# Kernel tuning notes

Measured on AMD Instinct MI355X. Metric: run time of the kernel, lower is better.

Reference implementation:

```python
import jax, jax.numpy as jnp
import numpy as np

ANCHORS = np.array([[4.63,1.97,1.74],[6.93,2.51,2.84],[6.37,2.85,3.19],[10.5,2.94,3.47],
                    [12.29,2.9,3.87],[0.5,2.53,0.98],[2.11,0.77,1.47],[1.7,0.6,1.28],
                    [0.73,0.67,1.77],[0.41,0.41,1.07]], dtype=np.float32)  # [10,3] nuScenes anchor sizes
BINS = 20          # anchor_size_bins
TEXT_DIM = 3 * BINS
NUM_PROPOSALS = 200
NMS_K = 3


def _vector_values():
    la = np.log(ANCHORS)
    return np.linspace(la.min() - 0.1, la.max() - 0.1, BINS).astype(np.float32)


def _anchor_vecs_normed():
    # soft_relu_bin_vectors: soft-bin log-anchors into BINS bins per dim, dim-major flatten
    vals = _vector_values()
    inc = vals[1] - vals[0]
    la = np.log(ANCHORS)                                      # [10,3]
    v = np.clip((la[:, :, None] - vals[None, None, :]) / inc, 0.0, 1.0)  # [10,3,BINS]
    v = v.reshape(10, TEXT_DIM)
    return (v / (1e-8 + np.linalg.norm(v, axis=1, keepdims=True))).astype(np.float32)


def conv2d(x, w, b=None):
    y = jax.lax.conv_general_dilated(x, w, (1, 1), 'SAME',
                                     dimension_numbers=('NCHW', 'OIHW', 'NCHW'))
    if b is not None:
        y = y + b[None, :, None, None]
    return y


def iou_sim_vec(a):
    # vectorized form of the triple-nested loop: prod over dims of min/max ratio
    mn = jnp.minimum(a[:, None, :], a[None, :, :])
    mx = jnp.maximum(a[:, None, :], a[None, :, :])
    return jnp.prod(mn / mx, axis=-1)                         # [10,10]


def setup_inputs() -> dict:
    key = jax.random.key(0)
    ks = jax.random.split(key, 8)
    B, Cin, hid, H, W = 2, 512, 128, 180, 180
    feats = jax.random.normal(ks[0], (B, Cin, H, W), jnp.float32)
    w_shared = jax.random.normal(ks[1], (hid, Cin, 3, 3), jnp.float32) * 0.02
    b_shared = jnp.zeros((hid,), jnp.float32)
    w_bb = jax.random.normal(ks[2], (hid, hid, 3, 3), jnp.float32) * 0.05
    gamma_bb = jnp.ones((hid,), jnp.float32)
    beta_bb = jnp.zeros((hid,), jnp.float32)
    w_hm = jax.random.normal(ks[3], (TEXT_DIM, hid, 3, 3), jnp.float32) * 0.05
    b_hm = jnp.zeros((TEXT_DIM,), jnp.float32)
    thr_scale = jnp.ones((1,), jnp.float32)                   # Threshold2d scale
    logit_scale = jnp.ones((1,), jnp.float32) * np.log(1.0 / 0.07)
    logit_bias = jnp.ones((1,), jnp.float32) * (-10.0)
    w_enc = jax.random.normal(ks[4], (hid, 3), jnp.float32) * 0.1  # Conv1d(3->hid, k=1)
    anchor_vecs = jnp.asarray(_anchor_vecs_normed())
    xs = jnp.arange(W, dtype=jnp.float32) + 0.5
    ys = jnp.arange(H, dtype=jnp.float32) + 0.5
    gy, gx = jnp.meshgrid(ys, xs, indexing='ij')
    bev_pos = jnp.stack([gx.reshape(-1), gy.reshape(-1)], axis=-1)  # [H*W, 2]
    return dict(feats=feats, w_shared=w_shared, b_shared=b_shared, w_bb=w_bb,
                gamma_bb=gamma_bb, beta_bb=beta_bb, w_hm=w_hm, b_hm=b_hm,
                thr_scale=thr_scale, logit_scale=logit_scale, logit_bias=logit_bias,
                w_enc=w_enc, anchor_vecs=anchor_vecs, bev_pos=bev_pos)


def reference(feats, w_shared, b_shared, w_bb, gamma_bb, beta_bb, w_hm, b_hm,
              thr_scale, logit_scale, logit_bias, w_enc, anchor_vecs, bev_pos):
    B, _, H, W = feats.shape
    # shared conv
    lidar_feat = conv2d(feats, w_shared, b_shared)            # [B,hid,H,W]
    # BasicBlock2D: conv + (inference) BN + ReLU
    x = conv2d(lidar_feat, w_bb)
    x = jax.nn.relu(x * gamma_bb[None, :, None, None] + beta_bb[None, :, None, None])
    # heatmap conv -> Threshold2d (sigmoid((x - thresholds) * scale))
    vec = conv2d(x, w_hm, b_hm)                               # [B,60,H,W]
    thresholds = jnp.asarray(np.tile(_vector_values(), 3))[None, :, None, None]
    vec = jax.nn.sigmoid((vec - thresholds) * thr_scale[0])
    # cosine sim vs normalized anchor bin-vectors -> per-class heatmap
    vecn = vec / (1e-8 + jnp.linalg.norm(vec, axis=1, keepdims=True))
    sim = jnp.einsum('bchw,kc->bkhw', vecn, anchor_vecs)      # [B,10,H,W]
    heatmap = jax.nn.sigmoid(logit_scale[0] * sim + logit_bias[0])
    # NMS: keep only local maxima within nms_kernel_size window
    local_max = jax.lax.reduce_window(heatmap, -jnp.inf, jax.lax.max,
                                      (1, 1, NMS_K, NMS_K), (1, 1, 1, 1), 'SAME')
    hm_nms = jnp.where(heatmap == local_max, heatmap, 0.0)
    # top-k proposals over classes x positions
    flat = hm_nms.reshape(B, -1)                              # [B, 10*H*W]
    top_scores, top_idx = jax.lax.top_k(flat, NUM_PROPOSALS)
    top_labels = top_idx // (H * W)                           # [B,P]
    top_pos = top_idx % (H * W)                               # [B,P]
    # gather proposal features, heatmap scores and bev positions
    hid = lidar_feat.shape[1]
    lidar_flat = lidar_feat.reshape(B, hid, H * W)
    idx_f = jnp.broadcast_to(top_pos[:, None, :], (B, hid, NUM_PROPOSALS))
    query_feat = jnp.take_along_axis(lidar_flat, idx_f, axis=2)  # [B,hid,P]
    hm_flat = heatmap.reshape(B, 10, H * W)
    idx_h = jnp.broadcast_to(top_pos[:, None, :], (B, 10, NUM_PROPOSALS))
    query_hm_score = jnp.take_along_axis(hm_flat, idx_h, axis=2)  # [B,10,P]
    query_pos = bev_pos[top_pos]                              # [B,P,2]
    # anchor value encoding (Conv1d(3->hid,k=1) on log-anchor sizes of top classes)
    top_anchor = jnp.log(jnp.asarray(ANCHORS))[top_labels]    # [B,P,3]
    query_feat = query_feat + jnp.einsum('cd,bpd->bcp', w_enc, top_anchor)
    sims = iou_sim_vec(jnp.asarray(ANCHORS))                  # [10,10] anchor IoU similarity
    return heatmap, top_scores, top_labels, query_feat, query_pos, query_hm_score, sims
```

## Files before the change

### kernel.cpp

```cpp
#include <hip/hip_runtime.h>
#include <math.h>


#define HW 180
#define NPIX 32400
#define NCLS 10
#define NPROP 200
#define HID 128
#define TDIM 60
#define NBIG (NCLS*NPIX)

#define TH_LO  (-0.9915981193)
#define TH_STEP (0.1789675812)

__constant__ float c_anchors[10][3] = {
  {4.63f,1.97f,1.74f},{6.93f,2.51f,2.84f},{6.37f,2.85f,3.19f},{10.5f,2.94f,3.47f},
  {12.29f,2.9f,3.87f},{0.5f,2.53f,0.98f},{2.11f,0.77f,1.47f},{1.7f,0.6f,1.28f},
  {0.73f,0.67f,1.77f},{0.41f,0.41f,1.07f}};

using f16x8 = _Float16 __attribute__((ext_vector_type(8)));
using f16x4 = _Float16 __attribute__((ext_vector_type(4)));
using f32x4 = float    __attribute__((ext_vector_type(4)));

#define GLD_LDS16(g, l) __builtin_amdgcn_global_load_lds( \
    (__attribute__((address_space(1))) void*)(g), \
    (__attribute__((address_space(3))) void*)(l), 16, 0, 0)

__device__ __forceinline__ void w_tr(const float* __restrict__ w, _Float16* __restrict__ dst,
                                     int CIN, int KS, int HALVES, int cout, int i) {
  int N = HALVES * KS * 36864;
  if (i >= N) return;
  int j = i & 7;
  int lane = (i >> 3) & 63;
  int mf = (i >> 9) & 3;
  int rest = i >> 11;
  int tsl = rest % 9; rest /= 9;
  int t = (tsl % 3) * 3 + (tsl / 3);
  int plane = rest & 1; rest >>= 1;
  int ks = rest % KS; int h = rest / KS;
  int co = h * 64 + mf * 16 + (lane & 15);
  int ch = ks * 32 + (lane >> 4) * 8 + j;
  float v = (co < cout) ? w[((size_t)co * CIN + ch) * 9 + t] : 0.f;
  _Float16 hi = (_Float16)v;
  dst[i] = plane ? (_Float16)(v - (float)hi) : hi;
}

__global__ __launch_bounds__(256)
void prep_kernel(const float* __restrict__ w_shared, const float* __restrict__ w_bb,
                 const float* __restrict__ w_hm, const float* __restrict__ feats,
                 _Float16* __restrict__ W1, _Float16* __restrict__ W2,
                 _Float16* __restrict__ W3, _Float16* __restrict__ X1,
                 float* __restrict__ out_sims, int* __restrict__ cnt) {
  int bid = blockIdx.x;
  const int tid = threadIdx.x;
  if (bid < 4608) { w_tr(w_shared, W1, 512, 16, 2, 128, bid * 256 + tid); return; }
  bid -= 4608;
  if (bid < 1152) { w_tr(w_bb, W2, 128, 4, 2, 128, bid * 256 + tid); return; }
  bid -= 1152;
  if (bid < 576)  { w_tr(w_hm, W3, 128, 4, 1, 60, bid * 256 + tid); return; }
  bid -= 576;
  if (bid < 4064) {
    int px = (bid % 127) * 256 + tid;
    int bks = bid / 127; int b = bks >> 4; int ks = bks & 15;
    if (px >= NPIX) return;
    const float* src = feats + ((size_t)(b * 512 + ks * 32)) * NPIX + px;
    float v[32];
#pragma unroll
    for (int c = 0; c < 32; ++c) v[c] = src[(size_t)c * NPIX];
    f16x8 hv[4], lv[4];
#pragma unroll
    for (int c = 0; c < 32; ++c) {
      _Float16 h = (_Float16)v[c];
      hv[c >> 3][c & 7] = h;
      lv[c >> 3][c & 7] = (_Float16)(v[c] - (float)h);
    }
    size_t ob = ((size_t)(b * 16 + ks) * NPIX + px) * 32;
#pragma unroll
    for (int i = 0; i < 4; ++i) {
      *(f16x8*)(X1 + ob + i * 8) = hv[i];
      *(f16x8*)(X1 + 33177600u + ob + i * 8) = lv[i];
    }
    return;
  }
  if (tid < 100) {
    int i = tid / 10, j = tid % 10;
    float r = 1.f;
#pragma unroll
    for (int d = 0; d < 3; ++d) {
      float ai = c_anchors[i][d], aj = c_anchors[j][d];
      r *= fminf(ai, aj) / fmaxf(ai, aj);
    }
    out_sims[tid] = r;
  }
  if (tid == 128) { cnt[0] = 0; cnt[1] = 0; }
}

template<int KS, int EPI>
__global__ __launch_bounds__(256, 2)
void conv_mfma(const _Float16* __restrict__ X, const _Float16* __restrict__ W,
               const float* __restrict__ p0, const float* __restrict__ p1,
               float* __restrict__ out0, _Float16* __restrict__ outX,
               const float* __restrict__ thr_scale, const float* __restrict__ logit_scale,
               const float* __restrict__ logit_bias, const float* __restrict__ anchor_vecs) {
  constexpr unsigned XPS = 2u * KS * NPIX * 32;
  constexpr bool DBUF = (EPI != 2);
  extern __shared__ _Float16 dlds[];
  _Float16* lds_x = dlds;
  _Float16* wA = dlds + 16128;
  _Float16* wB = dlds + 28416;
  float* lds_av = (float*)(dlds + 28416);

  const int hwid = blockIdx.x + 12 * blockIdx.y + 180 * blockIdx.z;
  const int xk = hwid & 7, xj = hwid >> 3;
  int zz, ii;
  if (EPI != 2) { zz = xk >> 1; ii = (xk & 1) * 90 + xj; }
  else          { zz = xk >> 2; ii = (xk & 3) * 45 + xj; }
  const int x0 = (ii % 12) * 16;
  const int y0 = (ii / 12) * 12;
  const int b  = (EPI == 2) ? zz : (zz >> 1);
  const int h  = (EPI == 2) ? 0 : (zz & 1);

  const int tid = threadIdx.x;
  const int wave = tid >> 6;
  const int lane = tid & 63;
  const int xl = lane & 15, kg = lane >> 4;

  {
    unsigned* p = (unsigned*)lds_x;
    for (int i = tid; i < 8064; i += 256) p[i] = 0u;
    if (EPI == 2)
      for (int i = tid; i < 600; i += 256) lds_av[i] = anchor_vecs[i];
  }

  unsigned offs[8]; unsigned okb = 0;
#pragma unroll
  for (int s = 0; s < 8; ++s) {
    int inst = wave + 4 * s;
    int c = inst * 64 + lane;
    bool valid = (c < 2016);
    int plane = (c >= 1008) ? 1 : 0;
    int cc = c - plane * 1008;
    int px = cc >> 2, q = cc & 3;
    int r = px / 18, xx = px - r * 18;
    int gy = y0 - 1 + r, gx = x0 - 1 + xx;
    bool ok = valid && ((unsigned)gy < 180u) && ((unsigned)gx < 180u);
    offs[s] = ok ? ((unsigned)((b * KS) * NPIX + gy * 180 + gx) * 32u + (unsigned)q * 8u
                    + (unsigned)plane * XPS) : 0u;
    okb |= (ok ? 1u : 0u) << s;
  }

  f32x4 acc[4][3];
#pragma unroll
  for (int mf = 0; mf < 4; ++mf)
#pragma unroll
    for (int f = 0; f < 3; ++f) acc[mf][f] = (f32x4){0.f, 0.f, 0.f, 0.f};

  auto COMPUTE = [&](int g, const _Float16* wbuf) {
    f16x8 bfh[5], bfl[5];
#pragma unroll
    for (int rr = 0; rr < 5; ++rr) {
      int lo = ((3 * wave + rr) * 18 + xl + g) * 32 + kg * 8;
      bfh[rr] = *(const f16x8*)(lds_x + lo);
      bfl[rr] = *(const f16x8*)(lds_x + 8064 + lo);
    }
    __builtin_amdgcn_s_setprio(1);
#pragma unroll
    for (int ky = 0; ky < 3; ++ky) {
      const _Float16* wt = wbuf + ky * 2048 + lane * 8;
      f16x8 ah[4], al[4];
#pragma unroll
      for (int mf = 0; mf < 4; ++mf) {
        ah[mf] = *(const f16x8*)(wt + mf * 512);
        al[mf] = *(const f16x8*)(wt + 6144 + mf * 512);
      }
#pragma unroll
      for (int mf = 0; mf < 4; ++mf)
#pragma unroll
        for (int f = 0; f < 3; ++f) {
          acc[mf][f] = __builtin_amdgcn_mfma_f32_16x16x32_f16(ah[mf], bfh[f + ky], acc[mf][f], 0, 0, 0);
          acc[mf][f] = __builtin_amdgcn_mfma_f32_16x16x32_f16(ah[mf], bfl[f + ky], acc[mf][f], 0, 0, 0);
          acc[mf][f] = __builtin_amdgcn_mfma_f32_16x16x32_f16(al[mf], bfh[f + ky], acc[mf][f], 0, 0, 0);
        }
    }
    __builtin_amdgcn_s_setprio(0);
  };
  auto WDMA = [&](const _Float16* gw, int g, _Float16* wbuf) {
#pragma unroll
    for (int s = 0; s < 6; ++s) {
      int c2 = wave + 4 * s;
      int pl = c2 / 12, idx = c2 - pl * 12;
      GLD_LDS16(gw + pl * 18432 + g * 6144 + idx * 512 + lane * 8,
                wbuf + pl * 6144 + idx * 512);
    }
  };
  auto XDMA = [&](unsigned kof) {
#pragma unroll
    for (int s = 0; s < 8; ++s) {
      if (okb & (1u << s))
        GLD_LDS16(X + (size_t)(offs[s] + kof), lds_x + (wave + 4 * s) * 512);
    }
  };

  const _Float16* gwb = W + (size_t)(h * KS) * 36864;
  for (int ks = 0; ks < KS; ++ks) {
    const unsigned kof = (unsigned)ks * (NPIX * 32u);
    const _Float16* gw = gwb + (size_t)ks * 36864;
    if (DBUF) {
      __syncthreads();
      XDMA(kof);
      WDMA(gw, 0, wA);
      __syncthreads();
      WDMA(gw, 1, wB);
      COMPUTE(0, wA);
      __syncthreads();
      WDMA(gw, 2, wA);
      COMPUTE(1, wB);
      __syncthreads();
      COMPUTE(2, wA);
    } else {
#pragma unroll
      for (int g = 0; g < 3; ++g) {
        __syncthreads();
        if (g == 0) XDMA(kof);
        WDMA(gw, g, wA);
        __syncthreads();
        COMPUTE(g, wA);
      }
    }
  }

  const int x = x0 + xl;
  if (EPI != 2) {
    if (x >= HW) return;
#pragma unroll
    for (int mf = 0; mf < 4; ++mf) {
      const int cobase = h * 64 + mf * 16 + kg * 4;
      f32x4 q0 = *(const f32x4*)(p0 + cobase);
      f32x4 q1 = (EPI == 1) ? *(const f32x4*)(p1 + cobase) : (f32x4){0.f,0.f,0.f,0.f};
#pragma unroll
      for (int f = 0; f < 3; ++f) {
        const int y = y0 + 3 * wave + f;
        const int kso = cobase >> 5, c32 = cobase & 31;
        size_t nidx = ((size_t)(b * 4 + kso) * NPIX + (size_t)y * 180 + x) * 32 + c32;
        if (EPI == 0) {
          f32x4 v;
          f16x4 h4, l4;
#pragma unroll
          for (int r = 0; r < 4; ++r) {
            float z = acc[mf][f][r] + q0[r];
            v[r] = z;
            _Float16 hh = (_Float16)z;
            h4[r] = hh;
            l4[r] = (_Float16)(z - (float)hh);
          }
          *(f32x4*)(out0 + nidx) = v;
          *(f16x4*)(outX + nidx) = h4;
          *(f16x4*)(outX + 8294400u + nidx) = l4;
        } else {
          f16x4 h4, l4;
#pragma unroll
          for (int r = 0; r < 4; ++r) {
            float z = fmaf(acc[mf][f][r], q0[r], q1[r]);
            z = fmaxf(z, 0.f);
            _Float16 hh = (_Float16)z;
            h4[r] = hh;
            l4[r] = (_Float16)(z - (float)hh);
          }
          *(f16x4*)(outX + nidx) = h4;
          *(f16x4*)(outX + 8294400u + nidx) = l4;
        }
      }
    }
  } else {
    const float s  = thr_scale[0];
    const float ls = logit_scale[0];
    const float lb = logit_bias[0];
    float bh4[4][4], th4[4][4];
    bool vmask[4];
#pragma unroll
    for (int mf = 0; mf < 4; ++mf) {
      const int cb = mf * 16 + kg * 4;
      vmask[mf] = (cb < TDIM);
#pragma unroll
      for (int r = 0; r < 4; ++r) {
        bh4[mf][r] = vmask[mf] ? p0[cb + r] : 0.f;
        th4[mf][r] = (float)(TH_LO + (double)((cb + r) % 20) * TH_STEP);
      }
    }
#pragma unroll
    for (int f = 0; f < 3; ++f) {
      const int y = y0 + 3 * wave + f;
      float v[4][4];
      float s2 = 0.f;
#pragma unroll
      for (int mf = 0; mf < 4; ++mf)
#pragma unroll
        for (int r = 0; r < 4; ++r) {
          float z = acc[mf][f][r] + bh4[mf][r];
          float t = (z - th4[mf][r]) * s;
          float vv = vmask[mf] ? 1.f / (1.f + expf(-t)) : 0.f;
          v[mf][r] = vv;
          s2 = fmaf(vv, vv, s2);
        }
      s2 += __shfl_xor(s2, 16);
      s2 += __shfl_xor(s2, 32);
      const float rs = 1.f / (1e-8f + sqrtf(s2));
      float hm[10];
#pragma unroll
      for (int k = 0; k < 10; ++k) {
        float d = 0.f;
#pragma unroll
        for (int mf = 0; mf < 4; ++mf) {
          const int cb = mf * 16 + kg * 4;
          f32x4 a = vmask[mf] ? *(const f32x4*)(lds_av + k * TDIM + cb)
                              : (f32x4){0.f, 0.f, 0.f, 0.f};
#pragma unroll
          for (int r = 0; r < 4; ++r) d = fmaf(v[mf][r], a[r], d);
        }
        d += __shfl_xor(d, 16);
        d += __shfl_xor(d, 32);
        hm[k] = 1.f / (1.f + expf(-fmaf(ls, d * rs, lb)));
      }
      if (x < HW) {
#pragma unroll
        for (int j = 0; j < 3; ++j) {
          int k = kg + 4 * j;
          if (k < NCLS)
            out0[((size_t)(b * NCLS + k) * HW + y) * HW + x] = hm[k];
        }
      }
    }
  }
}

__global__ __launch_bounds__(256)
void nms_kernel(const float* __restrict__ hm, float* __restrict__ ckey,
                int* __restrict__ cidx, int* __restrict__ cnt) {
  __shared__ int lcnt[2];
  __shared__ int lbase[2];
  const int tid = threadIdx.x;
  if (tid < 2) lcnt[tid] = 0;
  __syncthreads();

  int i = blockIdx.x * 256 + tid;
  bool surv = false; float v = 0.f; int bk = 0, p = 0;
  if (i < 2 * NBIG) {
    int x = i % HW; int y = (i / HW) % HW; int plane = i / NPIX;
    v = hm[i];
    float m = v;
#pragma unroll
    for (int dy = -1; dy <= 1; ++dy)
#pragma unroll
      for (int dx = -1; dx <= 1; ++dx) {
        int yy = y + dy, xx = x + dx;
        if ((unsigned)yy < (unsigned)HW && (unsigned)xx < (unsigned)HW)
          m = fmaxf(m, hm[((size_t)plane * NPIX) + yy * HW + xx]);
      }
    if (v == m) {
      surv = true;
      bk = i / NBIG;
      p = atomicAdd(&lcnt[bk], 1);
    }
  }
  __syncthreads();
  if (tid < 2 && lcnt[tid] > 0)
    lbase[tid] = atomicAdd(&cnt[tid], lcnt[tid]);
  __syncthreads();
  if (surv) {
    int slot = lbase[bk] + p;
    ckey[(size_t)bk * NBIG + slot] = v;
    cidx[(size_t)bk * NBIG + slot] = i - bk * NBIG;
  }
}

__global__ __launch_bounds__(1024)
void topk_kernel(const float* __restrict__ ckey, const int* __restrict__ cidx,
                 const int* __restrict__ cnt, const float* __restrict__ heatmap,
                 const float* __restrict__ bev_pos, float* __restrict__ out,
                 int* __restrict__ iws) {
  const int b = blockIdx.x;
  const int tid = threadIdx.x;
  const float* keys = ckey + (size_t)b * NBIG;
  const int* idxs = cidx + (size_t)b * NBIG;

  __shared__ unsigned hist[256];
  __shared__ unsigned sh_prefix;
  __shared__ int sh_want, sh_n;
  __shared__ int cntGT, cntTie;
  __shared__ unsigned gt_key[256], gt_idx[256];
  __shared__ unsigned tie_idx[2048];

  if (tid == 0) sh_n = cnt[b];
  __syncthreads();
  const int n = sh_n;

  unsigned prefix = 0; int want = NPROP;
  for (int shift = 24; shift >= 0; shift -= 8) {
    if (tid < 256) hist[tid] = 0u;
    __syncthreads();
    for (int i = tid; i < n; i += 1024) {
      unsigned k = __float_as_uint(keys[i]);
      bool match = (shift == 24) || ((k >> (shift + 8)) == (prefix >> (shift + 8)));
      if (match) atomicAdd(&hist[(k >> shift) & 255], 1u);
    }
    __syncthreads();
    if (tid == 0) {
      int cum = 0; int bsel = 0; sh_want = want;
      for (int bin = 255; bin >= 0; --bin) {
        cum += (int)hist[bin];
        if (cum >= want) { bsel = bin; sh_want = want - (cum - (int)hist[bin]); break; }
      }
      sh_prefix = prefix | ((unsigned)bsel << shift);
      cntGT = 0; cntTie = 0;
    }
    __syncthreads();
    prefix = sh_prefix; want = sh_want;
    __syncthreads();
  }
  const unsigned T = prefix;

  for (int i = tid; i < n; i += 1024) {
    unsigned k = __float_as_uint(keys[i]);
    if (k > T) {
      int p = atomicAdd(&cntGT, 1);
      if (p < 256) { gt_key[p] = k; gt_idx[p] = (unsigned)idxs[i]; }
    } else if (k == T) {
      int p = atomicAdd(&cntTie, 1);
      if (p < 2048) tie_idx[p] = (unsigned)idxs[i];
    }
  }
  __syncthreads();
  const int nGT = min(cntGT, 256);
  const int nTie = min(cntTie, 2048);

  for (int i = tid; i < 256; i += 1024)
    if (i >= nGT) { gt_key[i] = 0u; gt_idx[i] = 0xFFFFFFFFu; }
  for (int i = tid; i < 2048; i += 1024)
    if (i >= nTie) tie_idx[i] = 0xFFFFFFFFu;
  __syncthreads();

  for (int k2 = 2; k2 <= 256; k2 <<= 1) {
    for (int j = k2 >> 1; j > 0; j >>= 1) {
      for (int i = tid; i < 256; i += 1024) {
        int ixj = i ^ j;
        if (ixj > i) {
          unsigned ka = gt_key[i], kb = gt_key[ixj];
          unsigned ia = gt_idx[i], ib = gt_idx[ixj];
          bool firstA = (ka > kb) || (ka == kb && ia < ib);
          bool up = ((i & k2) == 0);
          if (up ? !firstA : firstA) {
            gt_key[i] = kb; gt_key[ixj] = ka;
            gt_idx[i] = ib; gt_idx[ixj] = ia;
          }
        }
      }
      __syncthreads();
    }
  }
  for (int k2 = 2; k2 <= 2048; k2 <<= 1) {
    for (int j = k2 >> 1; j > 0; j >>= 1) {
      for (int i = tid; i < 2048; i += 1024) {
        int ixj = i ^ j;
        if (ixj > i) {
          unsigned ia = tie_idx[i], ib = tie_idx[ixj];
          bool firstA = ia < ib;
          bool up = ((i & k2) == 0);
          if (up ? !firstA : firstA) { tie_idx[i] = ib; tie_idx[ixj] = ia; }
        }
      }
      __syncthreads();
    }
  }

  for (int r = tid; r < NPROP; r += 1024) {
    unsigned idx; float score;
    if (r < nGT) { idx = gt_idx[r]; score = __uint_as_float(gt_key[r]); }
    else         { idx = tie_idx[r - nGT]; score = __uint_as_float(T); }
    int label = (int)(idx / NPIX);
    int pos = (int)(idx - (unsigned)label * NPIX);
    out[648000 + b * NPROP + r] = score;
    out[648400 + b * NPROP + r] = (float)label;
    out[700000 + (b * NPROP + r) * 2 + 0] = bev_pos[pos * 2 + 0];
    out[700000 + (b * NPROP + r) * 2 + 1] = bev_pos[pos * 2 + 1];
#pragma unroll
    for (int k = 0; k < NCLS; ++k)
      out[700800 + (b * NCLS + k) * NPROP + r] = heatmap[(size_t)(b * NCLS + k) * NPIX + pos];
    iws[b * NPROP + r] = pos;
    iws[2 * NPROP + b * NPROP + r] = label;
  }
}

__global__ void gather_qf_kernel(const float* __restrict__ lidar, const float* __restrict__ w_enc,
                                 const int* __restrict__ iws, float* __restrict__ out_qf) {
  int p = blockIdx.x % NPROP;
  int b = blockIdx.x / NPROP;
  int c = threadIdx.x;
  int pos = iws[b * NPROP + p];
  int label = iws[2 * NPROP + b * NPROP + p];
  float la0 = logf(c_anchors[label][0]);
  float la1 = logf(c_anchors[label][1]);
  float la2 = logf(c_anchors[label][2]);
  float dot = w_enc[c * 3 + 0] * la0 + w_enc[c * 3 + 1] * la1 + w_enc[c * 3 + 2] * la2;
  float g = lidar[((size_t)(b * 4 + (c >> 5)) * NPIX + pos) * 32 + (c & 31)];
  out_qf[((size_t)b * HID + c) * NPROP + p] = g + dot;
}

extern "C" void kernel_launch(void* const* d_in, const int* in_sizes, int n_in,
                              void* d_out, int out_size, void* d_ws, size_t ws_size,
                              hipStream_t stream) {
  (void)in_sizes; (void)n_in; (void)out_size; (void)ws_size;
  const float* feats       = (const float*)d_in[0];
  const float* w_shared    = (const float*)d_in[1];
  const float* b_shared    = (const float*)d_in[2];
  const float* w_bb        = (const float*)d_in[3];
  const float* gamma_bb    = (const float*)d_in[4];
  const float* beta_bb     = (const float*)d_in[5];
  const float* w_hm        = (const float*)d_in[6];
  const float* b_hm        = (const float*)d_in[7];
  const float* thr_scale   = (const float*)d_in[8];
  const float* logit_scale = (const float*)d_in[9];
  const float* logit_bias  = (const float*)d_in[10];
  const float* w_enc       = (const float*)d_in[11];
  const float* anchor_vecs = (const float*)d_in[12];
  const float* bev_pos     = (const float*)d_in[13];
  float* out = (float*)d_out;

  float* ws = (float*)d_ws;
  size_t off = 0;
  _Float16* X1 = (_Float16*)(ws + off); off += 33177600;
  _Float16* X2 = (_Float16*)(ws + off); off += 8294400;
  float* lidarN = ws + off; off += 8294400;
  _Float16* X3 = (_Float16*)(ws + off); off += 8294400;
  _Float16* W1 = (_Float16*)(ws + off); off += 589824;
  _Float16* W2 = (_Float16*)(ws + off); off += 147456;
  _Float16* W3 = (_Float16*)(ws + off); off += 73728;
  float* ckey  = ws + off; off += (size_t)2 * NBIG;
  int*   cidx  = (int*)(ws + off); off += (size_t)2 * NBIG;
  int*   iws   = (int*)(ws + off); off += 800;
  int*   cnt   = (int*)(ws + off);

  prep_kernel<<<10401, 256, 0, stream>>>(w_shared, w_bb, w_hm, feats,
                                         W1, W2, W3, X1, out + 704800, cnt);

  const unsigned CONV_LDS = 81408;
  const unsigned HEAD_LDS = 59232;
  dim3 cgrid(12, 15, 4);
  conv_mfma<16,0><<<cgrid, 256, CONV_LDS, stream>>>(X1, W1, b_shared, nullptr, lidarN, X2,
                                                    nullptr, nullptr, nullptr, nullptr);
  conv_mfma<4, 1><<<cgrid, 256, CONV_LDS, stream>>>(X2, W2, gamma_bb, beta_bb, nullptr, X3,
                                                    nullptr, nullptr, nullptr, nullptr);
  dim3 hgrid(12, 15, 2);
  conv_mfma<4, 2><<<hgrid, 256, HEAD_LDS, stream>>>(X3, W3, b_hm, nullptr, out, nullptr,
                                                    thr_scale, logit_scale, logit_bias,
                                                    anchor_vecs);

  nms_kernel<<<(2*NBIG + 255)/256, 256, 0, stream>>>(out, ckey, cidx, cnt);
  topk_kernel<<<2, 1024, 0, stream>>>(ckey, cidx, cnt, out, bev_pos, out, iws);
  gather_qf_kernel<<<2*NPROP, 128, 0, stream>>>(lidarN, w_enc, iws, out + 648800);
}
```

Measured before the change: 516.6 us.

## Software-pipeline next k-slice input and weight DMA under last group's MFMAs

Restructures the double-buffered conv main loop so the activation tile and first weight group for the next K-slice are issued while the current slice's third weight group is being multiplied. The third group's LDS activation fragments are hoisted into registers before the barrier so the shared activation buffer can be overwritten. Weight buffers ping-pong across iterations instead of being reset each slice. This removes one barrier-separated load stall per slice, at the cost of extra register pressure from the hoisted fragments and more delicate synchronization.

```diff
diff --git a/kernel.cpp b/kernel.cpp
--- a/kernel.cpp
+++ b/kernel.cpp
@@ -155,14 +155,15 @@
 #pragma unroll
     for (int f = 0; f < 3; ++f) acc[mf][f] = (f32x4){0.f, 0.f, 0.f, 0.f};
 
-  auto COMPUTE = [&](int g, const _Float16* wbuf) {
-    f16x8 bfh[5], bfl[5];
+  auto HOIST = [&](int g, f16x8* bfh, f16x8* bfl) {
 #pragma unroll
     for (int rr = 0; rr < 5; ++rr) {
       int lo = ((3 * wave + rr) * 18 + xl + g) * 32 + kg * 8;
       bfh[rr] = *(const f16x8*)(lds_x + lo);
       bfl[rr] = *(const f16x8*)(lds_x + 8064 + lo);
     }
+  };
+  auto MFMAG = [&](const _Float16* wbuf, const f16x8* bfh, const f16x8* bfl) {
     __builtin_amdgcn_s_setprio(1);
 #pragma unroll
     for (int ky = 0; ky < 3; ++ky) {
@@ -183,6 +184,11 @@
         }
     }
     __builtin_amdgcn_s_setprio(0);
+  };
+  auto COMPUTE = [&](int g, const _Float16* wbuf) {
+    f16x8 bfh[5], bfl[5];
+    HOIST(g, bfh, bfl);
+    MFMAG(wbuf, bfh, bfl);
   };
   auto WDMA = [&](const _Float16* gw, int g, _Float16* wbuf) {
 #pragma unroll
@@ -202,22 +208,35 @@
   };
 
   const _Float16* gwb = W + (size_t)(h * KS) * 36864;
-  for (int ks = 0; ks < KS; ++ks) {
-    const unsigned kof = (unsigned)ks * (NPIX * 32u);
-    const _Float16* gw = gwb + (size_t)ks * 36864;
-    if (DBUF) {
+  if (DBUF) {
+    XDMA(0);
+    WDMA(gwb, 0, wA);
+    __syncthreads();
+    _Float16* Pm = wA;
+    _Float16* Qm = wB;
+    for (int ks = 0; ks < KS; ++ks) {
+      const _Float16* gw = gwb + (size_t)ks * 36864;
+      WDMA(gw, 1, Qm);
+      COMPUTE(0, Pm);
       __syncthreads();
-      XDMA(kof);
-      WDMA(gw, 0, wA);
+      WDMA(gw, 2, Pm);
+      COMPUTE(1, Qm);
       __syncthreads();
-      WDMA(gw, 1, wB);
-      COMPUTE(0, wA);
+      f16x8 bh2[5], bl2[5];
+      HOIST(2, bh2, bl2);
       __syncthreads();
-      WDMA(gw, 2, wA);
-      COMPUTE(1, wB);
-      __syncthreads();
-      COMPUTE(2, wA);
-    } else {
+      if (ks + 1 < KS) {
+        XDMA((unsigned)(ks + 1) * (NPIX * 32u));
+        WDMA(gw + 36864, 0, Qm);
+      }
+      MFMAG(Pm, bh2, bl2);
+      if (ks + 1 < KS) __syncthreads();
+      _Float16* t = Pm; Pm = Qm; Qm = t;
+    }
+  } else {
+    for (int ks = 0; ks < KS; ++ks) {
+      const unsigned kof = (unsigned)ks * (NPIX * 32u);
+      const _Float16* gw = gwb + (size_t)ks * 36864;
 #pragma unroll
       for (int g = 0; g < 3; ++g) {
         __syncthreads();
```

Result: no change. 513.9 us (-0.5%).
